# Performance work log

Hardware: AMD Instinct MI355X
Metric: run time of the kernel (lower is better)

The kernel has to match this reference:

```python
import jax, jax.numpy as jnp
import numpy as np

B, T, W, HP = 1, 64, 88, 48   # batch, frames, pitches, hidden_per_pitch
NU, NH, K = 24, 4, 25          # n_unit, n_heads, neighborhood window
HD = NU // NH                  # head dim = 6
HL = NU // 2                   # LSTM hidden per direction = 12


def _lstm_bidir(x, w_ih, w_hh, b_ih, b_hh):
    # x: [N, T, In]; w_ih: [2, 4*HL, In]; w_hh: [2, 4*HL, HL]; biases: [2, 4*HL]
    N = x.shape[0]
    def run(Wih, Whh, bih, bhh, reverse):
        def step(carry, xt):
            h, c = carry
            g = xt @ Wih.T + h @ Whh.T + bih + bhh
            i, f, gg, o = jnp.split(g, 4, axis=-1)  # torch gate order i,f,g,o
            c = jax.nn.sigmoid(f) * c + jax.nn.sigmoid(i) * jnp.tanh(gg)
            h = jax.nn.sigmoid(o) * jnp.tanh(c)
            return (h, c), h
        init = (jnp.zeros((N, HL), x.dtype), jnp.zeros((N, HL), x.dtype))
        _, ys = jax.lax.scan(step, init, jnp.swapaxes(x, 0, 1), reverse=reverse)
        return jnp.swapaxes(ys, 0, 1)
    return jnp.concatenate([run(w_ih[0], w_hh[0], b_ih[0], b_hh[0], False),
                            run(w_ih[1], w_hh[1], b_ih[1], b_hh[1], True)], axis=-1)


def _natten2d(x, qkv_w, qkv_b, rpb, proj_w, proj_b):
    # Neighborhood attention over 2D grid [B, Hh, Ww] with KxK window clamped at borders.
    Bn, Hh, Ww, C = x.shape
    qkv = (x @ qkv_w.T + qkv_b).reshape(Bn, Hh, Ww, 3, NH, HD)
    q = qkv[..., 0, :, :] * (HD ** -0.5)
    k = qkv[..., 1, :, :]
    v = qkv[..., 2, :, :]
    half = K // 2
    ar = jnp.arange(K)
    idx_i = jnp.clip(jnp.arange(Hh) - half, 0, Hh - K)[:, None] + ar  # [Hh,K]
    idx_j = jnp.clip(jnp.arange(Ww) - half, 0, Ww - K)[:, None] + ar  # [Ww,K]
    kg = k[:, idx_i][:, :, :, idx_j]  # [B,Hh,K,Ww,K,NH,HD]
    vg = v[:, idx_i][:, :, :, idx_j]
    ri = idx_i - jnp.arange(Hh)[:, None] + (K - 1)  # relative pos bias indices [Hh,K]
    rj = idx_j - jnp.arange(Ww)[:, None] + (K - 1)  # [Ww,K]
    bias = rpb[:, ri][:, :, :, rj]                  # [NH,Hh,K,Ww,K]
    logits = jnp.einsum('bijnd,biajcnd->bnijac', q, kg)
    logits = logits + jnp.transpose(bias, (0, 1, 3, 2, 4))[None]
    attn = jax.nn.softmax(logits.reshape(Bn, NH, Hh, Ww, K * K), axis=-1)
    attn = attn.reshape(Bn, NH, Hh, Ww, K, K)
    out = jnp.einsum('bnijac,biajcnd->bijnd', attn, vg).reshape(Bn, Hh, Ww, C)
    return out @ proj_w.T + proj_b


def _forward(features, condition, mask, emb, w_ih_l0, w_hh_l0, b_ih_l0, b_hh_l0,
             w_ih_l1, w_hh_l1, b_ih_l1, b_hh_l1, qkv_w, qkv_b, rpb, proj_w, proj_b,
             out_w, out_b):
    # concat: [B,T,88,HP] + [B,T,88,4] + [B,T,88,1] -> [B,T,88,HP+5]
    cat = jnp.concatenate([jnp.transpose(features, (0, 1, 3, 2)), emb[condition],
                           mask[..., None]], axis=-1)
    x = jnp.transpose(cat, (0, 2, 1, 3)).reshape(B * W, T, HP + 5)  # pitchwise LSTM
    x = _lstm_bidir(x, w_ih_l0, w_hh_l0, b_ih_l0, b_hh_l0)
    x = _lstm_bidir(x, w_ih_l1, w_hh_l1, b_ih_l1, b_hh_l1)
    x = jnp.transpose(x.reshape(B, W, T, NU), (0, 2, 1, 3))  # [B,T,88,NU]
    for _ in range(2):  # n_layers=2; Sequential(*[m]*2) => SHARED weights
        x = _natten2d(x, qkv_w, qkv_b, rpb, proj_w, proj_b)
    return x @ out_w.T + out_b  # [B,T,88,5]


def setup_inputs():
    ks = jax.random.split(jax.random.key(0), 24)
    def unif(k, shape, fan):
        s = 1.0 / np.sqrt(fan)
        return jax.random.uniform(k, shape, jnp.float32, -s, s)
    return {
        'features': jax.random.normal(ks[0], (B, T, HP, W), jnp.float32),
        'condition': jax.random.randint(ks[1], (B, T, W), 0, 5),
        'mask': jax.random.uniform(ks[2], (B, T, W), jnp.float32),
        'emb': jax.random.normal(ks[3], (5, 4), jnp.float32),
        'w_ih_l0': unif(ks[4], (2, 4 * HL, HP + 5), HL),
        'w_hh_l0': unif(ks[5], (2, 4 * HL, HL), HL),
        'b_ih_l0': unif(ks[6], (2, 4 * HL), HL),
        'b_hh_l0': unif(ks[7], (2, 4 * HL), HL),
        'w_ih_l1': unif(ks[8], (2, 4 * HL, 2 * HL), HL),
        'w_hh_l1': unif(ks[9], (2, 4 * HL, HL), HL),
        'b_ih_l1': unif(ks[10], (2, 4 * HL), HL),
        'b_hh_l1': unif(ks[11], (2, 4 * HL), HL),
        'qkv_w': unif(ks[12], (3 * NU, NU), NU),
        'qkv_b': unif(ks[13], (3 * NU,), NU),
        'rpb': jax.random.normal(ks[14], (NH, 2 * K - 1, 2 * K - 1), jnp.float32) * 0.02,
        'proj_w': unif(ks[15], (NU, NU), NU),
        'proj_b': unif(ks[16], (NU,), NU),
        'out_w': unif(ks[17], (5, NU), NU),
        'out_b': unif(ks[18], (5,), NU),
    }


def reference(features, condition, mask, emb, w_ih_l0, w_hh_l0, b_ih_l0, b_hh_l0,
              w_ih_l1, w_hh_l1, b_ih_l1, b_hh_l1, qkv_w, qkv_b, rpb, proj_w, proj_b,
              out_w, out_b):
    return _forward(features, condition, mask, emb, w_ih_l0, w_hh_l0, b_ih_l0, b_hh_l0,
                    w_ih_l1, w_hh_l1, b_ih_l1, b_hh_l1, qkv_w, qkv_b, rpb,
                    proj_w, proj_b, out_w, out_b)
```

## Files before the change

kernel.cpp:

```cpp
#include <hip/hip_runtime.h>
#include <hip/hip_bf16.h>

#define NPIX (64*88)
#define NSEQ 88
#define TT 64
#define F0 53
#define GATES 48
#define LOG2E 1.4426950408889634f

typedef __hip_bfloat16 bf16;

__device__ __forceinline__ float frcp(float x){ return __builtin_amdgcn_rcpf(x); }
__device__ __forceinline__ float fexp2(float x){ return __builtin_amdgcn_exp2f(x); }
__device__ __forceinline__ float blo(unsigned u){ return __uint_as_float(u<<16); }
__device__ __forceinline__ float bhi(unsigned u){ return __uint_as_float(u & 0xffff0000u); }

__device__ __forceinline__ float rl(float v, int l){
  return __int_as_float(__builtin_amdgcn_readlane(__float_as_int(v), l));
}
template<int K> __device__ __forceinline__ float qbcast(float v){
  constexpr int ctrl = K | (K<<2) | (K<<4) | (K<<6);
  return __int_as_float(__builtin_amdgcn_update_dpp(0, __float_as_int(v), ctrl, 0xf, 0xf, true));
}

template<int CTRL> __device__ __forceinline__ float dpp_add(float v){
  return v + __int_as_float(__builtin_amdgcn_update_dpp(0, __float_as_int(v), CTRL, 0xf, 0xf, true));
}
template<int CTRL> __device__ __forceinline__ float dpp_max(float v){
  int vi = __float_as_int(v);
  return fmaxf(v, __int_as_float(__builtin_amdgcn_update_dpp(vi, vi, CTRL, 0xf, 0xf, false)));
}
__device__ __forceinline__ float wred_sum(float v){
  v = dpp_add<0x111>(v); v = dpp_add<0x112>(v); v = dpp_add<0x114>(v); v = dpp_add<0x118>(v);
  v = dpp_add<0x142>(v); v = dpp_add<0x143>(v);
  return rl(v,63);
}
__device__ __forceinline__ float wred_max(float v){
  v = dpp_max<0x111>(v); v = dpp_max<0x112>(v); v = dpp_max<0x114>(v); v = dpp_max<0x118>(v);
  v = dpp_max<0x142>(v); v = dpp_max<0x143>(v);
  return rl(v,63);
}

__device__ __forceinline__ void lstm_dir(const float* __restrict__ whh,
    const float* gb_base, float* ybuf, int d, int lane){
  int u = lane >> 2, grp = lane & 3;
  int uc = (u < 12) ? u : 11;
  int j = grp*12 + uc;
  float w[12];
  const float* wb = whh + (d*GATES + j)*12;
  #pragma unroll
  for (int m=0;m<12;++m) w[m] = wb[m]*LOG2E;
  float negs = (grp==2) ? -2.f : -1.f;
  float amul = (grp==2) ?  2.f :  1.f;
  float aadd = (grp==2) ? -1.f :  0.f;
  const float* gb = gb_base + (d*TT)*49 + j;
  float hval = 0.f, cval = 0.f;
  int t0 = d ? (TT-1) : 0;
  float gnext = gb[t0*49];
  bool wr = (grp==0) && (u < 12);
  for (int s=0;s<TT;++s){
    int t = d ? (TT-1-s) : s;
    float gg = gnext;
    int tn = d ? max(TT-2-s,0) : min(s+1,TT-1);
    gnext = gb[tn*49];
    float h0=rl(hval,0),  h1=rl(hval,4),  h2=rl(hval,8),   h3=rl(hval,12);
    float h4=rl(hval,16), h5=rl(hval,20), h6=rl(hval,24),  h7=rl(hval,28);
    float h8=rl(hval,32), h9=rl(hval,36), h10=rl(hval,40), h11=rl(hval,44);
    float a0 = gg + h0*w[0] + h4*w[4] + h8*w[8];
    float a1 = h1*w[1] + h5*w[5] + h9*w[9];
    float a2 = h2*w[2] + h6*w[6] + h10*w[10];
    float a3 = h3*w[3] + h7*w[7] + h11*w[11];
    float dot = (a0+a1)+(a2+a3);
    float act = amul*frcp(1.f + fexp2(negs*dot)) + aadd;
    float ai = qbcast<0>(act);
    float af = qbcast<1>(act);
    float ag = qbcast<2>(act);
    float ao = qbcast<3>(act);
    float cn = af*cval + ai*ag;
    float th = 2.f*frcp(1.f + fexp2(-2.885390081777927f*cn)) - 1.f;
    hval = ao*th; cval = cn;
    if (wr) ybuf[t*25 + d*12 + u] = hval;
  }
}

__global__ __launch_bounds__(1024, 4) void k_core(
    const float* __restrict__ feat, const int* __restrict__ cond,
    const float* __restrict__ mask, const float* __restrict__ emb,
    const float* __restrict__ wih0, const float* __restrict__ whh0,
    const float* __restrict__ bih0, const float* __restrict__ bhh0,
    const float* __restrict__ wih1, const float* __restrict__ whh1,
    const float* __restrict__ bih1, const float* __restrict__ bhh1,
    const float* __restrict__ qkv_w, const float* __restrict__ qkv_b,
    float* __restrict__ q, bf16* __restrict__ kh, bf16* __restrict__ vh){
  int n = (blockIdx.x & 7)*11 + (blockIdx.x >> 3);
  int tid = threadIdx.x;
  int wave = tid >> 6; int lane = tid & 63;
  __shared__ float smem[12864];
  float* gbuf = smem;
  float* sx   = smem + 6272;
  float* y0   = smem + 6272+3392;
  float* y1   = smem + 6272+4992;
  float* outb = smem;

  for (int idx = tid; idx < TT*F0; idx += 1024){
    int t = idx / F0, f = idx - t*F0;
    float v;
    if (f < 48)      v = feat[(t*48 + f)*88 + n];
    else if (f < 52) v = emb[cond[t*88+n]*4 + (f-48)];
    else             v = mask[t*88+n];
    sx[idx] = v;
  }
  __syncthreads();

  {
    int wu = __builtin_amdgcn_readfirstlane(wave);
    int dd = wu >> 3, jg = wu & 7;
    const float* w0 = wih0 + (dd*GATES + jg*6)*F0;
    const float* xr = sx + lane*F0;
    float a0[6], a1[6];
    #pragma unroll
    for (int k=0;k<6;++k){
      int j = dd*GATES + jg*6 + k;
      a0[k] = bih0[j] + bhh0[j];
      a1[k] = 0.f;
    }
    #pragma unroll
    for (int f=0; f<52; f+=2){
      float x0 = xr[f], x1 = xr[f+1];
      #pragma unroll
      for (int k=0;k<6;++k){
        a0[k] += x0*w0[k*F0+f];
        a1[k] += x1*w0[k*F0+f+1];
      }
    }
    {
      float x0 = xr[52];
      #pragma unroll
      for (int k=0;k<6;++k) a0[k] += x0*w0[k*F0+52];
    }
    float* go = gbuf + (dd*TT + lane)*49 + jg*6;
    #pragma unroll
    for (int k=0;k<6;++k) go[k] = (a0[k] + a1[k])*LOG2E;
  }
  __syncthreads();

  if (wave < 2) lstm_dir(whh0, gbuf, y0, wave, lane);
  __syncthreads();

  {
    int wu = __builtin_amdgcn_readfirstlane(wave);
    int dd = wu >> 3, jg = wu & 7;
    const float* w1p = wih1 + (dd*GATES + jg*6)*24;
    const float* xr = y0 + lane*25;
    float a0[6], a1[6];
    #pragma unroll
    for (int k=0;k<6;++k){
      int j = dd*GATES + jg*6 + k;
      a0[k] = bih1[j] + bhh1[j];
      a1[k] = 0.f;
    }
    #pragma unroll
    for (int c=0; c<24; c+=2){
      float x0 = xr[c], x1 = xr[c+1];
      #pragma unroll
      for (int k=0;k<6;++k){
        a0[k] += x0*w1p[k*24+c];
        a1[k] += x1*w1p[k*24+c+1];
      }
    }
    float* go = gbuf + (dd*TT + lane)*49 + jg*6;
    #pragma unroll
    for (int k=0;k<6;++k) go[k] = (a0[k] + a1[k])*LOG2E;
  }
  __syncthreads();

  if (wave < 2) lstm_dir(whh1, gbuf, y1, wave, lane);
  __syncthreads();

  if (wave < 12){
    int wu = __builtin_amdgcn_readfirstlane(wave);
    int g0 = wu*6;
    const float* qw = qkv_w + g0*24;
    const float* xr = y1 + lane*25;
    float a0[6], a1[6];
    #pragma unroll
    for (int k=0;k<6;++k){ a0[k] = qkv_b[g0+k]; a1[k] = 0.f; }
    #pragma unroll
    for (int c=0; c<24; c+=2){
      float x0 = xr[c], x1 = xr[c+1];
      #pragma unroll
      for (int k=0;k<6;++k){
        a0[k] += x0*qw[k*24+c];
        a1[k] += x1*qw[k*24+c+1];
      }
    }
    float* oo = outb + lane*73 + g0;
    #pragma unroll
    for (int k=0;k<6;++k) oo[k] = a0[k] + a1[k];
  }
  __syncthreads();

  for (int idx = tid; idx < TT*72; idx += 1024){
    int gq = idx % 72; int t = idx / 72;
    int p = t*88 + n;
    float acc = outb[t*73 + gq];
    int s = gq/24, rem = gq - s*24;
    if (s==0) q[p*24+rem] = acc*0.4082482904638631f;
    else {
      int hh = rem/6, pos = rem - hh*6;
      bf16* dst = (s==1) ? kh : vh;
      dst[((size_t)hh*NPIX + p)*8 + pos] = __float2bfloat16(acc);
    }
  }
}

template<int MODE>
__global__ __launch_bounds__(512, 4) void k_natten(
    const float* __restrict__ q, const bf16* __restrict__ kh,
    const bf16* __restrict__ vh, const float* __restrict__ rpb,
    const float* __restrict__ pw, const float* __restrict__ pb,
    const float* __restrict__ qkv_w, const float* __restrict__ qkv_b,
    const float* __restrict__ ow, const float* __restrict__ ob,
    float* __restrict__ q2, bf16* __restrict__ kh2, bf16* __restrict__ vh2,
    float* __restrict__ out){
  int bid = blockIdx.x;
  int b = (bid & 7)*176 + (bid >> 3);
  int ti = b / 44, tj = b - ti*44;
  int i0 = ti*2, j0 = tj*2;
  int tid = threadIdx.x;
  int w = tid >> 6; int lane = tid & 63;
  int osi = min(max(i0-12,0),39);
  int osj = min(max(j0-12,0),63);

  __shared__ unsigned kv[16224];
  unsigned* kt = kv;
  unsigned* vt = kv + 8112;
  float* aop = (float*)kv;
  float* x4  = aop + 96;

  const uint4* kg = (const uint4*)kh;
  const uint4* vg = (const uint4*)vh;
  for (int idx = tid; idx < 2704; idx += 512){
    int h = idx / 676; int r = idx - h*676;
    int a = r / 26, cc = r - a*26;
    int gi = min(osi + a, 63), gj = min(osj + cc, 87);
    int src = h*NPIX + gi*88 + gj;
    uint4 kr = kg[src];
    uint4 vr = vg[src];
    int o = idx*3;
    kt[o] = kr.x; kt[o+1] = kr.y; kt[o+2] = kr.z;
    vt[o] = vr.x; vt[o+1] = vr.y; vt[o+2] = vr.z;
  }
  __syncthreads();

  int lrow = (lane >= 25 && lane < 50) ? 1 : 0;
  int lcc  = lane - (lane >= 50 ? 50 : (lane >= 25 ? 25 : 0));
  bool lact = lane < 50;

  float oacc[2][6];
  #pragma unroll
  for (int task=0; task<2; ++task){
    int tw = w + task*8;
    int px = tw & 3; int h = tw >> 2;
    int pi = i0 + (px>>1), pj = j0 + (px&1);
    int p = pi*88 + pj;
    int dsi = min(max(pi-12,0),39) - osi;
    int dsj = min(max(pj-12,0),63) - osj;
    int rbi = osi + dsi - pi + 24;
    int rbj = osj + dsj - pj + 24;
    const float* rpbh = rpb + (h*49 + rbi)*49 + rbj;
    int rowofs = h*2028 + (dsi*26 + dsj)*3;
    int lds0 = rowofs + (lrow*26 + lcc)*3;
    int rpo0 = lrow*49 + lcc;

    float qv[6];
    #pragma unroll
    for (int d=0; d<6; ++d) qv[d] = q[p*24 + h*6 + d];

    float lgv[13];
    float lmax = -1e30f;
    #pragma unroll
    for (int it=0; it<13; ++it){
      bool valid = lact && (it < 12 || lrow == 0);
      int r3 = lds0 + it*156;
      if (it == 12) r3 = lrow ? lds0 : r3;
      unsigned k0 = kt[r3], k1 = kt[r3+1], k2 = kt[r3+2];
      float lg = qv[0]*blo(k0)+qv[1]*bhi(k0)+qv[2]*blo(k1)
               + qv[3]*bhi(k1)+qv[4]*blo(k2)+qv[5]*bhi(k2);
      int ro = valid ? (rpo0 + it*98) : 0;
      lg += rpbh[ro];
      lg = valid ? lg : -1e30f;
      lgv[it] = lg;
      lmax = fmaxf(lmax, lg);
    }
    lmax = wred_max(lmax);
    float lsum = 0.f;
    #pragma unroll
    for (int it=0; it<13; ++it){
      float pe = __expf(lgv[it]-lmax);
      lgv[it] = pe; lsum += pe;
    }
    lsum = wred_sum(lsum);
    float acc[6] = {0,0,0,0,0,0};
    #pragma unroll
    for (int it=0; it<13; ++it){
      int r3 = lds0 + it*156;
      if (it == 12) r3 = lrow ? lds0 : r3;
      unsigned v0 = vt[r3], v1 = vt[r3+1], v2 = vt[r3+2];
      float pe = lgv[it];
      acc[0] += pe*blo(v0); acc[1] += pe*bhi(v0);
      acc[2] += pe*blo(v1); acc[3] += pe*bhi(v1);
      acc[4] += pe*blo(v2); acc[5] += pe*bhi(v2);
    }
    float inv = frcp(lsum);
    #pragma unroll
    for (int d=0; d<6; ++d) oacc[task][d] = wred_sum(acc[d])*inv;
  }

  __syncthreads();
  if (lane == 0){
    #pragma unroll
    for (int task=0; task<2; ++task){
      int tw = w + task*8;
      int px = tw & 3; int h = tw >> 2;
      #pragma unroll
      for (int d=0; d<6; ++d) aop[px*24 + h*6 + d] = oacc[task][d];
    }
  }
  __syncthreads();

  if (tid < 96){
    int pp = tid / 24, c = tid - (tid/24)*24;
    float a2 = pb[c];
    const float* wr = pw + c*24;
    #pragma unroll
    for (int k=0;k<24;++k) a2 += aop[pp*24+k]*wr[k];
    x4[pp*24+c] = a2;
  }
  __syncthreads();

  if (MODE == 0){
    if (tid < 288){
      int pp = tid / 72, g = tid - (tid/72)*72;
      float a2 = qkv_b[g];
      const float* wr = qkv_w + g*24;
      #pragma unroll
      for (int k=0;k<24;++k) a2 += x4[pp*24+k]*wr[k];
      int ppi = i0 + (pp>>1), ppj = j0 + (pp&1);
      int pp_ = ppi*88 + ppj;
      int s = g/24, rem = g - s*24;
      if (s==0) q2[pp_*24+rem] = a2*0.4082482904638631f;
      else {
        int hh = rem/6, pos = rem - hh*6;
        bf16* dst = (s==1) ? kh2 : vh2;
        dst[((size_t)hh*NPIX + pp_)*8 + pos] = __float2bfloat16(a2);
      }
    }
  } else {
    if (tid < 20){
      int pp = tid / 5, c = tid - (tid/5)*5;
      float a2 = ob[c];
      const float* wr = ow + c*24;
      #pragma unroll
      for (int k=0;k<24;++k) a2 += x4[pp*24+k]*wr[k];
      int ppi = i0 + (pp>>1), ppj = j0 + (pp&1);
      out[(ppi*88 + ppj)*5 + c] = a2;
    }
  }
}

extern "C" void kernel_launch(void* const* d_in, const int* in_sizes, int n_in,
                              void* d_out, int out_size, void* d_ws, size_t ws_size,
                              hipStream_t stream) {
  const float* feat    = (const float*)d_in[0];
  const int*   cond    = (const int*)  d_in[1];
  const float* mask    = (const float*)d_in[2];
  const float* emb     = (const float*)d_in[3];
  const float* w_ih_l0 = (const float*)d_in[4];
  const float* w_hh_l0 = (const float*)d_in[5];
  const float* b_ih_l0 = (const float*)d_in[6];
  const float* b_hh_l0 = (const float*)d_in[7];
  const float* w_ih_l1 = (const float*)d_in[8];
  const float* w_hh_l1 = (const float*)d_in[9];
  const float* b_ih_l1 = (const float*)d_in[10];
  const float* b_hh_l1 = (const float*)d_in[11];
  const float* qkv_w   = (const float*)d_in[12];
  const float* qkv_b   = (const float*)d_in[13];
  const float* rpb     = (const float*)d_in[14];
  const float* proj_w  = (const float*)d_in[15];
  const float* proj_b  = (const float*)d_in[16];
  const float* out_w   = (const float*)d_in[17];
  const float* out_b   = (const float*)d_in[18];
  float* out = (float*)d_out;

  float* ws  = (float*)d_ws;
  float* Q1  = ws;
  float* Q2  = Q1 + 135168;
  bf16*  KH1 = (bf16*)(Q2 + 135168);
  bf16*  VH1 = KH1 + 180224;
  bf16*  KH2 = VH1 + 180224;
  bf16*  VH2 = KH2 + 180224;

  k_core<<<NSEQ, 1024, 0, stream>>>(
      feat, cond, mask, emb,
      w_ih_l0, w_hh_l0, b_ih_l0, b_hh_l0,
      w_ih_l1, w_hh_l1, b_ih_l1, b_hh_l1,
      qkv_w, qkv_b, Q1, KH1, VH1);

  k_natten<0><<<8*176, 512, 0, stream>>>(
      Q1, KH1, VH1, rpb, proj_w, proj_b, qkv_w, qkv_b,
      nullptr, nullptr, Q2, KH2, VH2, nullptr);

  k_natten<1><<<8*176, 512, 0, stream>>>(
      Q2, KH2, VH2, rpb, proj_w, proj_b, nullptr, nullptr,
      out_w, out_b, nullptr, nullptr, nullptr, out);
}
```

Baseline: 184.1 us.

## Restructure neighborhood attention into per-head 8x8 tiles with online softmax

```diff
diff --git a/kernel.cpp b/kernel.cpp
--- a/kernel.cpp
+++ b/kernel.cpp
@@ -21,24 +21,6 @@
 template<int K> __device__ __forceinline__ float qbcast(float v){
   constexpr int ctrl = K | (K<<2) | (K<<4) | (K<<6);
   return __int_as_float(__builtin_amdgcn_update_dpp(0, __float_as_int(v), ctrl, 0xf, 0xf, true));
-}
-
-template<int CTRL> __device__ __forceinline__ float dpp_add(float v){
-  return v + __int_as_float(__builtin_amdgcn_update_dpp(0, __float_as_int(v), CTRL, 0xf, 0xf, true));
-}
-template<int CTRL> __device__ __forceinline__ float dpp_max(float v){
-  int vi = __float_as_int(v);
-  return fmaxf(v, __int_as_float(__builtin_amdgcn_update_dpp(vi, vi, CTRL, 0xf, 0xf, false)));
-}
-__device__ __forceinline__ float wred_sum(float v){
-  v = dpp_add<0x111>(v); v = dpp_add<0x112>(v); v = dpp_add<0x114>(v); v = dpp_add<0x118>(v);
-  v = dpp_add<0x142>(v); v = dpp_add<0x143>(v);
-  return rl(v,63);
-}
-__device__ __forceinline__ float wred_max(float v){
-  v = dpp_max<0x111>(v); v = dpp_max<0x112>(v); v = dpp_max<0x114>(v); v = dpp_max<0x118>(v);
-  v = dpp_max<0x142>(v); v = dpp_max<0x143>(v);
-  return rl(v,63);
 }
 
 __device__ __forceinline__ void lstm_dir(const float* __restrict__ whh,
@@ -214,158 +196,189 @@
   }
 }
 
-template<int MODE>
-__global__ __launch_bounds__(512, 4) void k_natten(
+__global__ __launch_bounds__(1024, 8) void k_nat(
     const float* __restrict__ q, const bf16* __restrict__ kh,
     const bf16* __restrict__ vh, const float* __restrict__ rpb,
-    const float* __restrict__ pw, const float* __restrict__ pb,
-    const float* __restrict__ qkv_w, const float* __restrict__ qkv_b,
-    const float* __restrict__ ow, const float* __restrict__ ob,
-    float* __restrict__ q2, bf16* __restrict__ kh2, bf16* __restrict__ vh2,
-    float* __restrict__ out){
+    float* __restrict__ ao){
   int bid = blockIdx.x;
-  int b = (bid & 7)*176 + (bid >> 3);
-  int ti = b / 44, tj = b - ti*44;
-  int i0 = ti*2, j0 = tj*2;
+  int h = bid / 88; int t = bid - h*88;
+  int ti = t / 11, tj = t - ti*11;
+  int i0 = ti*8, j0 = tj*8;
   int tid = threadIdx.x;
   int w = tid >> 6; int lane = tid & 63;
   int osi = min(max(i0-12,0),39);
   int osj = min(max(j0-12,0),63);
 
-  __shared__ unsigned kv[16224];
-  unsigned* kt = kv;
-  unsigned* vt = kv + 8112;
-  float* aop = (float*)kv;
-  float* x4  = aop + 96;
-
-  const uint4* kg = (const uint4*)kh;
-  const uint4* vg = (const uint4*)vh;
-  for (int idx = tid; idx < 2704; idx += 512){
-    int h = idx / 676; int r = idx - h*676;
-    int a = r / 26, cc = r - a*26;
-    int gi = min(osi + a, 63), gj = min(osj + cc, 87);
+  __shared__ unsigned lds[8609];
+  unsigned* kt = lds;
+  unsigned* vt = lds + 3104;
+  float*    rb = (float*)(lds + 6208);
+  float*  pbuf = (float*)lds;
+
+  {
+    int a = tid >> 5, b = tid & 31;
+    int gi = min(osi + a, 63), gj = min(osj + b, 87);
+    const uint4* kg = (const uint4*)kh;
+    const uint4* vg = (const uint4*)vh;
     int src = h*NPIX + gi*88 + gj;
     uint4 kr = kg[src];
     uint4 vr = vg[src];
-    int o = idx*3;
+    int o = a*97 + b*3;
     kt[o] = kr.x; kt[o+1] = kr.y; kt[o+2] = kr.z;
     vt[o] = vr.x; vt[o+1] = vr.y; vt[o+2] = vr.z;
   }
-  __syncthreads();
-
-  int lrow = (lane >= 25 && lane < 50) ? 1 : 0;
-  int lcc  = lane - (lane >= 50 ? 50 : (lane >= 25 ? 25 : 0));
-  bool lact = lane < 50;
-
-  float oacc[2][6];
+  for (int idx = tid; idx < 2401; idx += 1024){
+    rb[idx] = rpb[h*2401 + idx] * LOG2E;
+  }
+  __syncthreads();
+
+  int pi = i0 + (lane >> 3), pj = j0 + (lane & 7);
+  int p = pi*88 + pj;
+  int si = min(max(pi-12,0),39), sj = min(max(pj-12,0),63);
+  int kbase = (si - osi)*97 + (sj - osj)*3;
+  int rbase = (si - pi + 24)*49 + (sj - pj + 24);
+
+  float qv[6];
+  const float* qp = q + p*24 + h*6;
   #pragma unroll
-  for (int task=0; task<2; ++task){
-    int tw = w + task*8;
-    int px = tw & 3; int h = tw >> 2;
-    int pi = i0 + (px>>1), pj = j0 + (px&1);
-    int p = pi*88 + pj;
-    int dsi = min(max(pi-12,0),39) - osi;
-    int dsj = min(max(pj-12,0),63) - osj;
-    int rbi = osi + dsi - pi + 24;
-    int rbj = osj + dsj - pj + 24;
-    const float* rpbh = rpb + (h*49 + rbi)*49 + rbj;
-    int rowofs = h*2028 + (dsi*26 + dsj)*3;
-    int lds0 = rowofs + (lrow*26 + lcc)*3;
-    int rpo0 = lrow*49 + lcc;
-
-    float qv[6];
-    #pragma unroll
-    for (int d=0; d<6; ++d) qv[d] = q[p*24 + h*6 + d];
-
-    float lgv[13];
-    float lmax = -1e30f;
-    #pragma unroll
-    for (int it=0; it<13; ++it){
-      bool valid = lact && (it < 12 || lrow == 0);
-      int r3 = lds0 + it*156;
-      if (it == 12) r3 = lrow ? lds0 : r3;
-      unsigned k0 = kt[r3], k1 = kt[r3+1], k2 = kt[r3+2];
-      float lg = qv[0]*blo(k0)+qv[1]*bhi(k0)+qv[2]*blo(k1)
-               + qv[3]*bhi(k1)+qv[4]*blo(k2)+qv[5]*bhi(k2);
-      int ro = valid ? (rpo0 + it*98) : 0;
-      lg += rpbh[ro];
-      lg = valid ? lg : -1e30f;
-      lgv[it] = lg;
-      lmax = fmaxf(lmax, lg);
-    }
-    lmax = wred_max(lmax);
-    float lsum = 0.f;
-    #pragma unroll
-    for (int it=0; it<13; ++it){
-      float pe = __expf(lgv[it]-lmax);
-      lgv[it] = pe; lsum += pe;
-    }
-    lsum = wred_sum(lsum);
-    float acc[6] = {0,0,0,0,0,0};
-    #pragma unroll
-    for (int it=0; it<13; ++it){
-      int r3 = lds0 + it*156;
-      if (it == 12) r3 = lrow ? lds0 : r3;
-      unsigned v0 = vt[r3], v1 = vt[r3+1], v2 = vt[r3+2];
-      float pe = lgv[it];
-      acc[0] += pe*blo(v0); acc[1] += pe*bhi(v0);
-      acc[2] += pe*blo(v1); acc[3] += pe*bhi(v1);
-      acc[4] += pe*blo(v2); acc[5] += pe*bhi(v2);
-    }
-    float inv = frcp(lsum);
-    #pragma unroll
-    for (int d=0; d<6; ++d) oacc[task][d] = wred_sum(acc[d])*inv;
-  }
-
-  __syncthreads();
-  if (lane == 0){
-    #pragma unroll
-    for (int task=0; task<2; ++task){
-      int tw = w + task*8;
-      int px = tw & 3; int h = tw >> 2;
-      #pragma unroll
-      for (int d=0; d<6; ++d) aop[px*24 + h*6 + d] = oacc[task][d];
-    }
-  }
-  __syncthreads();
-
-  if (tid < 96){
-    int pp = tid / 24, c = tid - (tid/24)*24;
-    float a2 = pb[c];
+  for (int d=0; d<6; ++d) qv[d] = qp[d]*LOG2E;
+
+  float m2 = -1e30f, s = 0.f;
+  float acc[6] = {0,0,0,0,0,0};
+
+  int a = 0, b = w;
+  while (a < 25){
+    int o = kbase + a*97 + b*3;
+    unsigned k0 = kt[o], k1 = kt[o+1], k2 = kt[o+2];
+    float bias = rb[rbase + a*49 + b];
+    float lg = fmaf(qv[0], blo(k0), bias);
+    lg = fmaf(qv[1], bhi(k0), lg);
+    lg = fmaf(qv[2], blo(k1), lg);
+    lg = fmaf(qv[3], bhi(k1), lg);
+    lg = fmaf(qv[4], blo(k2), lg);
+    lg = fmaf(qv[5], bhi(k2), lg);
+    bool up = (lg - m2) > 8.f;
+    if (__any(up)){
+      float sc = up ? fexp2(m2 - lg) : 1.f;
+      s *= sc;
+      #pragma unroll
+      for (int d=0; d<6; ++d) acc[d] *= sc;
+      m2 = up ? lg : m2;
+    }
+    float pe = fexp2(lg - m2);
+    s += pe;
+    unsigned v0 = vt[o], v1 = vt[o+1], v2 = vt[o+2];
+    acc[0] += pe*blo(v0); acc[1] += pe*bhi(v0);
+    acc[2] += pe*blo(v1); acc[3] += pe*bhi(v1);
+    acc[4] += pe*blo(v2); acc[5] += pe*bhi(v2);
+    b += 16; if (b >= 25){ b -= 25; ++a; }
+  }
+
+  __syncthreads();
+  if (w > 0){
+    int pb = (w-1)*512 + lane;
+    pbuf[pb]      = m2;
+    pbuf[pb+64]   = s;
+    #pragma unroll
+    for (int d=0; d<6; ++d) pbuf[pb + (2+d)*64] = acc[d];
+  }
+  __syncthreads();
+  if (w == 0){
+    float M = m2, S = s;
+    float A[6];
+    #pragma unroll
+    for (int d=0; d<6; ++d) A[d] = acc[d];
+    #pragma unroll
+    for (int k=0; k<15; ++k){
+      int pb = k*512 + lane;
+      float mk = pbuf[pb];
+      float sk = pbuf[pb+64];
+      float Mn = fmaxf(M, mk);
+      float sc1 = fexp2(M - Mn);
+      float sc2 = fexp2(mk - Mn);
+      S = S*sc1 + sk*sc2;
+      #pragma unroll
+      for (int d=0; d<6; ++d)
+        A[d] = A[d]*sc1 + pbuf[pb + (2+d)*64]*sc2;
+      M = Mn;
+    }
+    float inv = frcp(S);
+    float* aop = ao + p*24 + h*6;
+    #pragma unroll
+    for (int d=0; d<6; ++d) aop[d] = A[d]*inv;
+  }
+}
+
+__global__ __launch_bounds__(1024) void k_ep0(const float* __restrict__ ao,
+    const float* __restrict__ pw, const float* __restrict__ pb,
+    const float* __restrict__ qkv_w, const float* __restrict__ qkv_b,
+    float* __restrict__ q2, bf16* __restrict__ kh2, bf16* __restrict__ vh2){
+  int p0 = blockIdx.x*64; int tid = threadIdx.x;
+  __shared__ float ar[64*25];
+  __shared__ float xr[64*25];
+  for (int idx = tid; idx < 64*24; idx += 1024){
+    int px = idx / 24, c = idx - px*24;
+    ar[px*25 + c] = ao[p0*24 + idx];
+  }
+  __syncthreads();
+  for (int idx = tid; idx < 64*24; idx += 1024){
+    int px = idx / 24, c = idx - px*24;
+    float acc = pb[c];
     const float* wr = pw + c*24;
-    #pragma unroll
-    for (int k=0;k<24;++k) a2 += aop[pp*24+k]*wr[k];
-    x4[pp*24+c] = a2;
-  }
-  __syncthreads();
-
-  if (MODE == 0){
-    if (tid < 288){
-      int pp = tid / 72, g = tid - (tid/72)*72;
-      float a2 = qkv_b[g];
-      const float* wr = qkv_w + g*24;
-      #pragma unroll
-      for (int k=0;k<24;++k) a2 += x4[pp*24+k]*wr[k];
-      int ppi = i0 + (pp>>1), ppj = j0 + (pp&1);
-      int pp_ = ppi*88 + ppj;
-      int s = g/24, rem = g - s*24;
-      if (s==0) q2[pp_*24+rem] = a2*0.4082482904638631f;
-      else {
-        int hh = rem/6, pos = rem - hh*6;
-        bf16* dst = (s==1) ? kh2 : vh2;
-        dst[((size_t)hh*NPIX + pp_)*8 + pos] = __float2bfloat16(a2);
-      }
-    }
-  } else {
-    if (tid < 20){
-      int pp = tid / 5, c = tid - (tid/5)*5;
-      float a2 = ob[c];
-      const float* wr = ow + c*24;
-      #pragma unroll
-      for (int k=0;k<24;++k) a2 += x4[pp*24+k]*wr[k];
-      int ppi = i0 + (pp>>1), ppj = j0 + (pp&1);
-      out[(ppi*88 + ppj)*5 + c] = a2;
-    }
+    const float* arow = ar + px*25;
+    #pragma unroll
+    for (int k=0;k<24;++k) acc += arow[k]*wr[k];
+    xr[px*25 + c] = acc;
+  }
+  __syncthreads();
+  for (int idx = tid; idx < 64*72; idx += 1024){
+    int px = idx / 72, g = idx - px*72;
+    float acc = qkv_b[g];
+    const float* wr = qkv_w + g*24;
+    const float* xrow = xr + px*25;
+    #pragma unroll
+    for (int k=0;k<24;++k) acc += xrow[k]*wr[k];
+    int p = p0 + px;
+    int sg = g/24, rem = g - sg*24;
+    if (sg==0) q2[p*24+rem] = acc*0.4082482904638631f;
+    else {
+      int hh = rem/6, pos = rem - hh*6;
+      bf16* dst = (sg==1) ? kh2 : vh2;
+      dst[((size_t)hh*NPIX + p)*8 + pos] = __float2bfloat16(acc);
+    }
+  }
+}
+
+__global__ __launch_bounds__(1024) void k_ep1(const float* __restrict__ ao,
+    const float* __restrict__ pw, const float* __restrict__ pb,
+    const float* __restrict__ ow, const float* __restrict__ ob,
+    float* __restrict__ out){
+  int p0 = blockIdx.x*64; int tid = threadIdx.x;
+  __shared__ float ar[64*25];
+  __shared__ float xr[64*25];
+  for (int idx = tid; idx < 64*24; idx += 1024){
+    int px = idx / 24, c = idx - px*24;
+    ar[px*25 + c] = ao[p0*24 + idx];
+  }
+  __syncthreads();
+  for (int idx = tid; idx < 64*24; idx += 1024){
+    int px = idx / 24, c = idx - px*24;
+    float acc = pb[c];
+    const float* wr = pw + c*24;
+    const float* arow = ar + px*25;
+    #pragma unroll
+    for (int k=0;k<24;++k) acc += arow[k]*wr[k];
+    xr[px*25 + c] = acc;
+  }
+  __syncthreads();
+  if (tid < 64*5){
+    int px = tid / 5, c = tid - px*5;
+    float acc = ob[c];
+    const float* wr = ow + c*24;
+    const float* xrow = xr + px*25;
+    #pragma unroll
+    for (int k=0;k<24;++k) acc += xrow[k]*wr[k];
+    out[(p0 + px)*5 + c] = acc;
   }
 }
 
@@ -396,7 +409,8 @@
   float* ws  = (float*)d_ws;
   float* Q1  = ws;
   float* Q2  = Q1 + 135168;
-  bf16*  KH1 = (bf16*)(Q2 + 135168);
+  float* AO  = Q2 + 135168;
+  bf16*  KH1 = (bf16*)(AO + 135168);
   bf16*  VH1 = KH1 + 180224;
   bf16*  KH2 = VH1 + 180224;
   bf16*  VH2 = KH2 + 180224;
@@ -407,11 +421,12 @@
       w_ih_l1, w_hh_l1, b_ih_l1, b_hh_l1,
       qkv_w, qkv_b, Q1, KH1, VH1);
 
-  k_natten<0><<<8*176, 512, 0, stream>>>(
-      Q1, KH1, VH1, rpb, proj_w, proj_b, qkv_w, qkv_b,
-      nullptr, nullptr, Q2, KH2, VH2, nullptr);
-
-  k_natten<1><<<8*176, 512, 0, stream>>>(
-      Q2, KH2, VH2, rpb, proj_w, proj_b, nullptr, nullptr,
-      out_w, out_b, nullptr, nullptr, nullptr, out);
-}
+  k_nat<<<4*88, 1024, 0, stream>>>(Q1, KH1, VH1, rpb, AO);
+
+  k_ep0<<<NPIX/64, 1024, 0, stream>>>(AO, proj_w, proj_b, qkv_w, qkv_b,
+      Q2, KH2, VH2);
+
+  k_nat<<<4*88, 1024, 0, stream>>>(Q2, KH2, VH2, rpb, AO);
+
+  k_ep1<<<NPIX/64, 1024, 0, stream>>>(AO, proj_w, proj_b, out_w, out_b, out);
+}
```

New measurement: 186.7 us. About the same (+1.4%).
